# Kernel optimization log

Hardware: AMD Instinct MI355X
Metric: run time of the kernel (lower is better)

The kernel has to match this reference:

```python
import jax, jax.numpy as jnp
import numpy as np
from jax import lax

H = 128; N = 32768; D = 16; B = 256; E2 = N * D; L = 2; NC = 10
NPG = N // B  # nodes per graph


def _ln(x, g, b):
    m = jnp.mean(x, -1, keepdims=True)
    v = jnp.mean((x - m) ** 2, -1, keepdims=True)
    return (x - m) * lax.rsqrt(v + 1e-5) * g + b


def _lrelu(x):
    return jnp.where(x >= 0, x, 0.01 * x)


def _seg_mean(x, ids):
    s = jax.ops.segment_sum(x, ids, num_segments=B)
    c = jax.ops.segment_sum(jnp.ones((x.shape[0], 1), x.dtype), ids, num_segments=B)
    return s / c


def _lstm_agg(seq, Wih, Whh, bih, bhh):
    # seq: [N, D, H] neighbor message sequences; returns final hidden [N, H]
    n = seq.shape[0]
    h0 = jnp.zeros((n, H), seq.dtype)

    def step(carry, x):
        h, c = carry
        g = x @ Wih.T + bih + h @ Whh.T + bhh  # [N, 4H], gate order i,f,g,o (torch LSTM)
        i, f, gg, o = jnp.split(g, 4, axis=-1)
        c = jax.nn.sigmoid(f) * c + jax.nn.sigmoid(i) * jnp.tanh(gg)
        h = jax.nn.sigmoid(o) * jnp.tanh(c)
        return (h, c), None

    (h, _), _ = lax.scan(step, (h0, h0), jnp.swapaxes(seq, 0, 1))
    return h


def _gru(x, h, Wih, Whh, bih, bhh):
    gi = x @ Wih.T + bih
    gh = h @ Whh.T + bhh
    ir, iz, inn = jnp.split(gi, 3, axis=-1)
    hr, hz, hn = jnp.split(gh, 3, axis=-1)
    r = jax.nn.sigmoid(ir + hr)
    z = jax.nn.sigmoid(iz + hz)
    nn_ = jnp.tanh(inn + r * hn)
    return (1.0 - z) * nn_ + z * h


def _sage(fs, fd, nbr, Wih, Whh, bih, bhh, fsW, fsb, fnW, fnb):
    # SAGEConv with LSTM aggregator: fc_self(dst) + fc_neigh(lstm over neighbor feats)
    hn = _lstm_agg(fs[nbr], Wih, Whh, bih, bhh)  # [N, H]
    return fd @ fsW.T + fsb + hn @ fnW.T + fnb


def _forward(ints, fl):
    (act_ids, dur_ids, act2_ids, nbr_a2d, nbr_d2a, src2, dst2, graph_ids) = ints
    (emb_act, emb_dur, emb_act2, transform_W, transform_b,
     ggc_W, ggc_b, gru_Wih, gru_Whh, gru_bih, gru_bhh, hn_g, hn_b,
     lstm_Wih, lstm_Whh, lstm_bih, lstm_bhh, fcs_W, fcs_b, fcn_W, fcn_b,
     n1_g, n1_b, n3_g, n3_b,
     mh_W1, mh_b1, mh_W2, mh_b2, mo_W1, mo_b1, mo_W2, mo_b2,
     mlp_W1, mlp_b1, mlp_W2, mlp_b2, cls_W, cls_b) = fl

    # embedding lookups (dropout layers are identity in eval mode)
    h_act = emb_act[act_ids]
    h_dur = emb_dur[dur_ids]
    h_g2 = emb_act2[act2_ids]
    h_new = jnp.concatenate([h_g2, h_dur], axis=1) @ transform_W.T + transform_b

    # homo branch: GatedGraphConv (n_steps=2, 1 etype) + residual + LN + leaky_relu
    res = h_new
    hh = h_new
    for _ in range(2):
        m = hh @ ggc_W.T + ggc_b
        a = jax.ops.segment_sum(m[src2], dst2, num_segments=N)
        hh = _gru(a, hh, gru_Wih, gru_Whh, gru_bih, gru_bhh)
    h_new = _lrelu(_ln(hh + res, hn_g, hn_b))
    hg2_mean = _seg_mean(h_new, graph_ids)  # [B, H]

    # hetero branch: L layers of HeteroGraphConv(SAGEConv lstm) + norms + residuals
    ha, hd = h_act, h_dur
    for l in range(L):
        nd = _sage(ha, hd, nbr_a2d, lstm_Wih[l, 0], lstm_Whh[l, 0], lstm_bih[l, 0], lstm_bhh[l, 0],
                   fcs_W[l, 0], fcs_b[l, 0], fcn_W[l, 0], fcn_b[l, 0])
        na = _sage(hd, ha, nbr_d2a, lstm_Wih[l, 1], lstm_Whh[l, 1], lstm_bih[l, 1], lstm_bhh[l, 1],
                   fcs_W[l, 1], fcs_b[l, 1], fcn_W[l, 1], fcn_b[l, 1])
        na = _lrelu(_ln(na, n1_g[l, 0], n1_b[l, 0]))
        nd = _lrelu(_ln(nd, n1_g[l, 1], n1_b[l, 1]))
        ha = _lrelu(_ln(ha + na, n3_g[l, 0], n3_b[l, 0]))
        hd = _lrelu(_ln(hd + nd, n3_g[l, 1], n3_b[l, 1]))
    hg_mean = _seg_mean(ha, graph_ids) + _seg_mean(hd, graph_ids)  # sum over ntypes

    o1 = jax.nn.relu(jax.nn.relu(hg2_mean @ mo_W1.T + mo_b1) @ mo_W2.T + mo_b2)
    o2 = jax.nn.relu(jax.nn.relu(hg_mean @ mh_W1.T + mh_b1) @ mh_W2.T + mh_b2)
    hc = jnp.concatenate([o1, hg2_mean, o2, hg_mean], axis=1)  # [B, 4H]
    preds = jax.nn.relu(jax.nn.relu(hc @ mlp_W1.T + mlp_b1) @ mlp_W2.T + mlp_b2)
    return preds @ cls_W.T + cls_b  # [B, NC]


def setup_inputs() -> dict:
    key = jax.random.key(0)
    ks = iter(jax.random.split(key, 48))
    s = 1.0 / np.sqrt(H)

    def nrm(shape, sc=s):
        return jax.random.normal(next(ks), shape, jnp.float32) * sc

    inp = {}
    inp['act_ids'] = jax.random.randint(next(ks), (N,), 0, 30)
    inp['dur_ids'] = jax.random.randint(next(ks), (N,), 0, 1024)
    inp['act2_ids'] = jax.random.randint(next(ks), (N,), 0, 30)
    inp['nbr_a2d'] = jax.random.randint(next(ks), (N, D), 0, N)
    inp['nbr_d2a'] = jax.random.randint(next(ks), (N, D), 0, N)
    inp['src2'] = jax.random.randint(next(ks), (E2,), 0, N)
    inp['dst2'] = jax.random.randint(next(ks), (E2,), 0, N)
    inp['graph_ids'] = jnp.arange(N) // NPG

    inp['emb_act'] = nrm((30, H))
    inp['emb_dur'] = nrm((1024, H))
    inp['emb_act2'] = nrm((30, H))
    inp['transform_W'] = nrm((H, 2 * H), 1.0 / np.sqrt(2 * H))
    inp['transform_b'] = jnp.zeros((H,), jnp.float32)
    inp['ggc_W'] = nrm((H, H))
    inp['ggc_b'] = jnp.zeros((H,), jnp.float32)
    inp['gru_Wih'] = nrm((3 * H, H))
    inp['gru_Whh'] = nrm((3 * H, H))
    inp['gru_bih'] = jnp.zeros((3 * H,), jnp.float32)
    inp['gru_bhh'] = jnp.zeros((3 * H,), jnp.float32)
    inp['hn_g'] = jnp.ones((H,), jnp.float32)
    inp['hn_b'] = jnp.zeros((H,), jnp.float32)
    inp['lstm_Wih'] = nrm((L, 2, 4 * H, H))
    inp['lstm_Whh'] = nrm((L, 2, 4 * H, H))
    inp['lstm_bih'] = jnp.zeros((L, 2, 4 * H), jnp.float32)
    inp['lstm_bhh'] = jnp.zeros((L, 2, 4 * H), jnp.float32)
    inp['fcs_W'] = nrm((L, 2, H, H))
    inp['fcs_b'] = jnp.zeros((L, 2, H), jnp.float32)
    inp['fcn_W'] = nrm((L, 2, H, H))
    inp['fcn_b'] = jnp.zeros((L, 2, H), jnp.float32)
    inp['n1_g'] = jnp.ones((L, 2, H), jnp.float32)
    inp['n1_b'] = jnp.zeros((L, 2, H), jnp.float32)
    inp['n3_g'] = jnp.ones((L, 2, H), jnp.float32)
    inp['n3_b'] = jnp.zeros((L, 2, H), jnp.float32)
    inp['mh_W1'] = nrm((H, H)); inp['mh_b1'] = jnp.zeros((H,), jnp.float32)
    inp['mh_W2'] = nrm((H, H)); inp['mh_b2'] = jnp.zeros((H,), jnp.float32)
    inp['mo_W1'] = nrm((H, H)); inp['mo_b1'] = jnp.zeros((H,), jnp.float32)
    inp['mo_W2'] = nrm((H, H)); inp['mo_b2'] = jnp.zeros((H,), jnp.float32)
    inp['mlp_W1'] = nrm((2 * H, 4 * H), 1.0 / np.sqrt(4 * H))
    inp['mlp_b1'] = jnp.zeros((2 * H,), jnp.float32)
    inp['mlp_W2'] = nrm((H, 2 * H), 1.0 / np.sqrt(2 * H))
    inp['mlp_b2'] = jnp.zeros((H,), jnp.float32)
    inp['cls_W'] = nrm((NC, H))
    inp['cls_b'] = jnp.zeros((NC,), jnp.float32)
    return inp


def reference(act_ids, dur_ids, act2_ids, nbr_a2d, nbr_d2a, src2, dst2, graph_ids,
              emb_act, emb_dur, emb_act2, transform_W, transform_b,
              ggc_W, ggc_b, gru_Wih, gru_Whh, gru_bih, gru_bhh, hn_g, hn_b,
              lstm_Wih, lstm_Whh, lstm_bih, lstm_bhh, fcs_W, fcs_b, fcn_W, fcn_b,
              n1_g, n1_b, n3_g, n3_b,
              mh_W1, mh_b1, mh_W2, mh_b2, mo_W1, mo_b1, mo_W2, mo_b2,
              mlp_W1, mlp_b1, mlp_W2, mlp_b2, cls_W, cls_b):
    ints = (act_ids, dur_ids, act2_ids, nbr_a2d, nbr_d2a, src2, dst2, graph_ids)
    fl = (emb_act, emb_dur, emb_act2, transform_W, transform_b,
          ggc_W, ggc_b, gru_Wih, gru_Whh, gru_bih, gru_bhh, hn_g, hn_b,
          lstm_Wih, lstm_Whh, lstm_bih, lstm_bhh, fcs_W, fcs_b, fcn_W, fcn_b,
          n1_g, n1_b, n3_g, n3_b,
          mh_W1, mh_b1, mh_W2, mh_b2, mo_W1, mo_b1, mo_W2, mo_b2,
          mlp_W1, mlp_b1, mlp_W2, mlp_b2, cls_W, cls_b)
    return _forward(ints, fl)
```

## Files before the change

kernel.cpp:

```cpp
#include <hip/hip_runtime.h>
#include <hip/hip_fp16.h>
#include <math.h>

#define NN 32768
#define HH 128
#define DD 16
#define BB 256
#define E2N (NN*DD)
#define NF (NN*HH)

typedef __attribute__((ext_vector_type(4))) float f32x4;
typedef __attribute__((ext_vector_type(4))) unsigned short u16x4;
typedef __attribute__((ext_vector_type(8))) unsigned short u16x8;
typedef _Float16 f16x8 __attribute__((ext_vector_type(8)));

__device__ __forceinline__ float fsig(float x) {
  return __builtin_amdgcn_rcpf(1.0f + __builtin_amdgcn_exp2f(-1.442695041f*x));
}
__device__ __forceinline__ float ftanh(float x) {
  return 1.0f - 2.0f*__builtin_amdgcn_rcpf(1.0f + __builtin_amdgcn_exp2f(2.885390082f*x));
}
__device__ __forceinline__ void hsplit(float x, unsigned short& h, unsigned short& l) {
  __half hh_ = __float2half_rn(x);
  h = __half_as_ushort(hh_);
  l = __half_as_ushort(__float2half_rn(x - __half2float(hh_)));
}

struct TDesc { const float* src; float* dst; int R; int C; };
struct TDescArr { TDesc d[8]; };

__global__ void transpose_many(TDescArr da) {
  TDesc t = da.d[blockIdx.y];
  int idx = blockIdx.x*256 + threadIdx.x;
  if (idx < t.R*t.C) {
    int r = idx / t.C, c = idx - r*t.C;
    t.dst[(size_t)c*t.R + r] = t.src[idx];
  }
}

__global__ void bias_sum_kernel(const float* __restrict__ bih, const float* __restrict__ bhh,
                                float* __restrict__ bsum) {
  int i = blockIdx.x*256 + threadIdx.x;
  if (i < 2048) bsum[i] = bih[i] + bhh[i];
}

__global__ void f32to16_kernel(const float* __restrict__ in, unsigned short* __restrict__ out) {
  int base = (blockIdx.x*256 + threadIdx.x) * 4;
  float4 v = *(const float4*)(in + base);
  u16x4 p;
  p[0] = __half_as_ushort(__float2half_rn(v.x));
  p[1] = __half_as_ushort(__float2half_rn(v.y));
  p[2] = __half_as_ushort(__float2half_rn(v.z));
  p[3] = __half_as_ushort(__float2half_rn(v.w));
  *(u16x4*)(out + base) = p;
}

__global__ void wsplit16_kernel(const float* __restrict__ W,
                                unsigned short* __restrict__ hi,
                                unsigned short* __restrict__ lo) {
  int i = blockIdx.x*256 + threadIdx.x;
  unsigned short h, l;
  hsplit(W[i], h, l);
  hi[i] = h; lo[i] = l;
}

__global__ void embed3_kernel(const int* __restrict__ a_ids, const int* __restrict__ d_ids,
                              const int* __restrict__ a2_ids,
                              const float* __restrict__ ea, const float* __restrict__ ed,
                              const float* __restrict__ ea2,
                              float* __restrict__ ha, float* __restrict__ hd,
                              float* __restrict__ hg2) {
  int idx = blockIdx.x*256 + threadIdx.x;
  int n = idx >> 7, j = idx & 127;
  int w = blockIdx.y;
  if (w == 0)      ha[idx]  = ea[(size_t)a_ids[n]*128 + j];
  else if (w == 1) hd[idx]  = ed[(size_t)d_ids[n]*128 + j];
  else             hg2[idx] = ea2[(size_t)a2_ids[n]*128 + j];
}

template<int BN, int ACT>
__global__ __launch_bounds__(256) void gemm_nt(
    const float* __restrict__ A0, const float* __restrict__ A1,
    const float* __restrict__ A2, const float* __restrict__ A3,
    int lda, const float* __restrict__ WT, const float* __restrict__ bias,
    float* __restrict__ C, int K, int beta)
{
  extern __shared__ float sm[];
  const int KP = K + 4;
  float* At = sm;
  float* Bc = sm + 32*KP;
  const int tid = threadIdx.x;
  const int m0 = blockIdx.x*32;
  const int ng = tid >> 5, cg = tid & 31;
  const int n0 = ng*4, c4 = cg*4;
  constexpr int G = BN/128;
  float acc[G][4][4];
#pragma unroll
  for (int g=0; g<G; ++g)
#pragma unroll
    for (int i=0;i<4;++i)
#pragma unroll
      for (int e=0;e<4;++e) acc[g][i][e] = 0.0f;

  const int nf4 = K >> 2;
  for (int idx = tid; idx < 32*nf4; idx += 256) {
    int row = idx / nf4;
    int kk = (idx - row*nf4) << 2;
    const float* Ap = (kk < 128) ? A0 : (kk < 256) ? A1 : (kk < 384) ? A2 : A3;
    float4 v = *(const float4*)(Ap + (size_t)(m0+row)*lda + (kk & 127));
    *(float4*)(At + row*KP + kk) = v;
  }
  const int nchunk = K >> 4;
  for (int kc = 0; kc < nchunk; ++kc) {
    __syncthreads();
    for (int idx = tid; idx < 16*(BN/4); idx += 256) {
      int kk = idx / (BN/4);
      int jq = idx - kk*(BN/4);
      *(float4*)(Bc + kk*BN + jq*4) = *(const float4*)(WT + (size_t)(kc*16+kk)*BN + jq*4);
    }
    __syncthreads();
    for (int k=0;k<16;++k) {
      const int kk = kc*16 + k;
      float av[4];
#pragma unroll
      for (int i=0;i<4;++i) av[i] = At[(n0+i)*KP + kk];
#pragma unroll
      for (int g=0; g<G; ++g) {
        float4 bv = *(const float4*)(Bc + k*BN + g*128 + c4);
        float bb[4] = {bv.x, bv.y, bv.z, bv.w};
#pragma unroll
        for (int i=0;i<4;++i)
#pragma unroll
          for (int e=0;e<4;++e)
            acc[g][i][e] += av[i]*bb[e];
      }
    }
  }
#pragma unroll
  for (int g=0; g<G; ++g) {
#pragma unroll
    for (int i=0;i<4;++i) {
      float* dst = C + (size_t)(m0+n0+i)*BN + g*128 + c4;
      float o[4];
#pragma unroll
      for (int e=0;e<4;++e) o[e] = acc[g][i][e];
      if (bias) {
#pragma unroll
        for (int e=0;e<4;++e) o[e] += bias[g*128 + c4 + e];
      }
      if (beta) {
        float4 p = *(const float4*)dst;
        o[0]+=p.x; o[1]+=p.y; o[2]+=p.z; o[3]+=p.w;
      }
      if (ACT==1) {
#pragma unroll
        for (int e=0;e<4;++e) o[e] = fmaxf(o[e], 0.0f);
      }
      *(float4*)dst = make_float4(o[0],o[1],o[2],o[3]);
    }
  }
}

__device__ __forceinline__ void stage_hi_lo(const float* __restrict__ A, int rb, int tid,
                                            unsigned short* xhi, unsigned short* xlo) {
  const int r = tid >> 3;
  const int cf = (tid & 7) * 16;
  const float* src = A + (size_t)(rb + r)*128 + cf;
  unsigned short* dh = xhi + r*136 + cf;
  unsigned short* dl = xlo + r*136 + cf;
#pragma unroll
  for (int q=0; q<4; ++q) {
    float4 v = *(const float4*)(src + q*4);
    float vs[4] = {v.x, v.y, v.z, v.w};
    u16x4 ph, pl;
#pragma unroll
    for (int e=0;e<4;++e){ unsigned short h_,l_; hsplit(vs[e],h_,l_); ph[e]=h_; pl[e]=l_; }
    *(u16x4*)(dh + q*4) = ph;
    *(u16x4*)(dl + q*4) = pl;
  }
}

__global__ __launch_bounds__(512) void mgemm(
    const float* __restrict__ A,
    const unsigned short* __restrict__ Whi, const unsigned short* __restrict__ Wlo,
    const float* __restrict__ bias, float* __restrict__ C, int BN, int ntpw)
{
  __shared__ unsigned short xhi[64*136];
  __shared__ unsigned short xlo[64*136];
  const int tid = threadIdx.x;
  const int w = tid >> 6;
  const int lane = tid & 63;
  const int ln16 = lane & 15;
  const int lq = lane >> 4;
  const int rb = blockIdx.x * 64;
  stage_hi_lo(A, rb, tid, xhi, xlo);
  __syncthreads();

  for (int j=0; j<ntpw; ++j) {
    const int tile = w + j*8;
    f32x4 acc[4];
    f32x4 bv = *(const f32x4*)(bias + tile*16 + lq*4);
#pragma unroll
    for (int nt=0; nt<4; ++nt) acc[nt] = bv;
#pragma unroll
    for (int kt=0; kt<4; ++kt) {
      const int bo = kt*32 + lq*8;
      f16x8 bxh[4], bxl[4];
#pragma unroll
      for (int nt=0; nt<4; ++nt) {
        bxh[nt] = *(const f16x8*)(xhi + (nt*16+ln16)*136 + bo);
        bxl[nt] = *(const f16x8*)(xlo + (nt*16+ln16)*136 + bo);
      }
      const size_t co = (size_t)(tile*16 + ln16)*128 + kt*32 + lq*8;
      f16x8 ah = *(const f16x8*)(Whi + co);
      f16x8 al = *(const f16x8*)(Wlo + co);
#pragma unroll
      for (int nt=0; nt<4; ++nt) {
        acc[nt] = __builtin_amdgcn_mfma_f32_16x16x32_f16(ah, bxh[nt], acc[nt], 0,0,0);
        acc[nt] = __builtin_amdgcn_mfma_f32_16x16x32_f16(ah, bxl[nt], acc[nt], 0,0,0);
        acc[nt] = __builtin_amdgcn_mfma_f32_16x16x32_f16(al, bxh[nt], acc[nt], 0,0,0);
      }
    }
#pragma unroll
    for (int nt=0; nt<4; ++nt) {
      f32x4 o = acc[nt];
      *(float4*)(C + (size_t)(rb + nt*16 + ln16)*BN + tile*16 + lq*4) =
          make_float4(o[0],o[1],o[2],o[3]);
    }
  }
}

__global__ __launch_bounds__(512) void mgemm2(
    const float* __restrict__ A1,
    const unsigned short* __restrict__ W1hi, const unsigned short* __restrict__ W1lo,
    const float* __restrict__ A2,
    const unsigned short* __restrict__ W2hi, const unsigned short* __restrict__ W2lo,
    const float* __restrict__ bias1, const float* __restrict__ bias2,
    float* __restrict__ C, int wstride)
{
  extern __shared__ unsigned short sm16[];
  unsigned short* x1hi = sm16;
  unsigned short* x1lo = sm16 + 8704;
  unsigned short* x2hi = sm16 + 17408;
  unsigned short* x2lo = sm16 + 26112;
  const int tid = threadIdx.x;
  const int w = tid >> 6;
  const int lane = tid & 63;
  const int ln16 = lane & 15;
  const int lq = lane >> 4;
  const int rb = blockIdx.x * 64;
  stage_hi_lo(A1, rb, tid, x1hi, x1lo);
  stage_hi_lo(A2, rb, tid, x2hi, x2lo);
  __syncthreads();

  f32x4 acc[4];
  {
    f32x4 bv = *(const f32x4*)(bias1 + w*16 + lq*4);
    if (bias2) {
      f32x4 b2 = *(const f32x4*)(bias2 + w*16 + lq*4);
#pragma unroll
      for (int e=0;e<4;++e) bv[e] += b2[e];
    }
#pragma unroll
    for (int nt=0; nt<4; ++nt) acc[nt] = bv;
  }
#pragma unroll
  for (int p=0; p<2; ++p) {
    const unsigned short* xh = p ? x2hi : x1hi;
    const unsigned short* xl = p ? x2lo : x1lo;
    const unsigned short* Wh = p ? W2hi : W1hi;
    const unsigned short* Wl = p ? W2lo : W1lo;
#pragma unroll
    for (int kt=0; kt<4; ++kt) {
      const int bo = kt*32 + lq*8;
      f16x8 bxh[4], bxl[4];
#pragma unroll
      for (int nt=0; nt<4; ++nt) {
        bxh[nt] = *(const f16x8*)(xh + (nt*16+ln16)*136 + bo);
        bxl[nt] = *(const f16x8*)(xl + (nt*16+ln16)*136 + bo);
      }
      const size_t co = (size_t)(w*16 + ln16)*wstride + kt*32 + lq*8;
      f16x8 ah = *(const f16x8*)(Wh + co);
      f16x8 al = *(const f16x8*)(Wl + co);
#pragma unroll
      for (int nt=0; nt<4; ++nt) {
        acc[nt] = __builtin_amdgcn_mfma_f32_16x16x32_f16(ah, bxh[nt], acc[nt], 0,0,0);
        acc[nt] = __builtin_amdgcn_mfma_f32_16x16x32_f16(ah, bxl[nt], acc[nt], 0,0,0);
        acc[nt] = __builtin_amdgcn_mfma_f32_16x16x32_f16(al, bxh[nt], acc[nt], 0,0,0);
      }
    }
  }
#pragma unroll
  for (int nt=0; nt<4; ++nt) {
    f32x4 o = acc[nt];
    *(float4*)(C + (size_t)(rb + nt*16 + ln16)*128 + w*16 + lq*4) =
        make_float4(o[0],o[1],o[2],o[3]);
  }
}

__global__ __launch_bounds__(512) void gru_fused(
    const float* __restrict__ abuf, float* __restrict__ hh,
    const unsigned short* __restrict__ GIhi, const unsigned short* __restrict__ GIlo,
    const unsigned short* __restrict__ GHhi, const unsigned short* __restrict__ GHlo,
    const float* __restrict__ bih, const float* __restrict__ bhh)
{
  extern __shared__ unsigned short sm16[];
  unsigned short* xhi = sm16;
  unsigned short* xlo = sm16 + 8704;
  unsigned short* hhi = sm16 + 17408;
  unsigned short* hlo = sm16 + 26112;
  const int tid = threadIdx.x;
  const int w = tid >> 6;
  const int lane = tid & 63;
  const int ln16 = lane & 15;
  const int lq = lane >> 4;
  const int rb = blockIdx.x * 64;
  stage_hi_lo(abuf, rb, tid, xhi, xlo);
  stage_hi_lo(hh, rb, tid, hhi, hlo);
  __syncthreads();

  f32x4 rr[4], zz[4], nn_[4];
#pragma unroll
  for (int j=0; j<3; ++j) {
    const int tile = w + j*8;
    f32x4 ai[4], ag[4];
    f32x4 bi = *(const f32x4*)(bih + tile*16 + lq*4);
    f32x4 bg = *(const f32x4*)(bhh + tile*16 + lq*4);
#pragma unroll
    for (int nt=0; nt<4; ++nt) { ai[nt] = bi; ag[nt] = bg; }
#pragma unroll
    for (int kt=0; kt<4; ++kt) {
      const int bo = kt*32 + lq*8;
      f16x8 bxh[4], bxl[4], bhh_[4], bhl_[4];
#pragma unroll
      for (int nt=0; nt<4; ++nt) {
        bxh[nt] = *(const f16x8*)(xhi + (nt*16+ln16)*136 + bo);
        bxl[nt] = *(const f16x8*)(xlo + (nt*16+ln16)*136 + bo);
        bhh_[nt] = *(const f16x8*)(hhi + (nt*16+ln16)*136 + bo);
        bhl_[nt] = *(const f16x8*)(hlo + (nt*16+ln16)*136 + bo);
      }
      const size_t co = (size_t)(tile*16 + ln16)*128 + kt*32 + lq*8;
      f16x8 ih = *(const f16x8*)(GIhi + co);
      f16x8 il = *(const f16x8*)(GIlo + co);
      f16x8 gh = *(const f16x8*)(GHhi + co);
      f16x8 gl = *(const f16x8*)(GHlo + co);
#pragma unroll
      for (int nt=0; nt<4; ++nt) {
        ai[nt] = __builtin_amdgcn_mfma_f32_16x16x32_f16(ih, bxh[nt], ai[nt], 0,0,0);
        ai[nt] = __builtin_amdgcn_mfma_f32_16x16x32_f16(ih, bxl[nt], ai[nt], 0,0,0);
        ai[nt] = __builtin_amdgcn_mfma_f32_16x16x32_f16(il, bxh[nt], ai[nt], 0,0,0);
        ag[nt] = __builtin_amdgcn_mfma_f32_16x16x32_f16(gh, bhh_[nt], ag[nt], 0,0,0);
        ag[nt] = __builtin_amdgcn_mfma_f32_16x16x32_f16(gh, bhl_[nt], ag[nt], 0,0,0);
        ag[nt] = __builtin_amdgcn_mfma_f32_16x16x32_f16(gl, bhh_[nt], ag[nt], 0,0,0);
      }
    }
#pragma unroll
    for (int nt=0; nt<4; ++nt) {
#pragma unroll
      for (int e=0; e<4; ++e) {
        if (j == 0)      rr[nt][e] = fsig(ai[nt][e] + ag[nt][e]);
        else if (j == 1) zz[nt][e] = fsig(ai[nt][e] + ag[nt][e]);
        else             nn_[nt][e] = ftanh(ai[nt][e] + rr[nt][e]*ag[nt][e]);
      }
    }
  }
#pragma unroll
  for (int nt=0; nt<4; ++nt) {
    float* hp = hh + (size_t)(rb + nt*16 + ln16)*128 + w*16 + lq*4;
    float4 ho = *(const float4*)hp;
    float hv[4] = {ho.x, ho.y, ho.z, ho.w};
    float o[4];
#pragma unroll
    for (int e=0; e<4; ++e)
      o[e] = (1.0f - zz[nt][e])*nn_[nt][e] + zz[nt][e]*hv[e];
    *(float4*)hp = make_float4(o[0],o[1],o[2],o[3]);
  }
}

__global__ __launch_bounds__(512) void lstm_fused6(
    float* __restrict__ hL,
    const unsigned short* __restrict__ fs16a, const unsigned short* __restrict__ fs16d,
    const int* __restrict__ nbrA, const int* __restrict__ nbrD,
    const unsigned short* __restrict__ WI0, const unsigned short* __restrict__ WH0,
    const unsigned short* __restrict__ WI1, const unsigned short* __restrict__ WH1,
    const float* __restrict__ bsum0, const float* __restrict__ bsum1)
{
  __shared__ unsigned short xb[64*132];
  __shared__ unsigned short hb[64*132];
  const int tid = threadIdx.x;
  const int w = tid >> 6;
  const int lane = tid & 63;
  const int ln16 = lane & 15;
  const int lq = lane >> 4;
  const int b = blockIdx.x;
  const bool dir = (b >= 512);
  const int nb = (dir ? (b - 512) : b) * 64;
  const unsigned short* fs16 = dir ? fs16d : fs16a;
  const int* nbr = dir ? nbrD : nbrA;
  const unsigned short* WI = dir ? WI1 : WI0;
  const unsigned short* WH = dir ? WH1 : WH0;
  const float* bsum = dir ? bsum1 : bsum0;

  const int gr = tid >> 3;
  const int gc = (tid & 7) * 16;
  const int* nrow = nbr + (size_t)(nb + gr)*DD;

  f32x4 bias[4];
#pragma unroll
  for (int g=0; g<4; ++g)
    bias[g] = *(const f32x4*)(bsum + g*128 + w*16 + lq*4);

  f32x4 cst[4];
#pragma unroll
  for (int nt=0; nt<4; ++nt)
#pragma unroll
    for (int e=0; e<4; ++e) cst[nt][e] = 0.0f;

  u16x8 xg0, xg1;
  {
    int gidx = nrow[0];
    const unsigned short* src = fs16 + (size_t)gidx*128 + gc;
    xg0 = *(const u16x8*)(src);
    xg1 = *(const u16x8*)(src + 8);
    unsigned short* d = xb + gr*132 + gc;
    *(u16x8*)d = xg0;
    *(u16x8*)(d+8) = xg1;
  }
  int gnext = nrow[1];

#pragma unroll 1
  for (int t=0; t<16; ++t) {
    __syncthreads();

    f32x4 racc[4][4];
#pragma unroll
    for (int g=0; g<4; ++g)
#pragma unroll
      for (int nt=0; nt<4; ++nt)
        racc[g][nt] = bias[g];

#pragma unroll
    for (int kt=0; kt<4; ++kt) {
      const int bo = kt*32 + lq*8;
      f16x8 bx[4];
#pragma unroll
      for (int nt=0; nt<4; ++nt)
        bx[nt] = *(const f16x8*)(xb + (nt*16+ln16)*132 + bo);
#pragma unroll
      for (int g=0; g<4; ++g) {
        f16x8 aI = *(const f16x8*)(WI + (size_t)(g*128 + w*16 + ln16)*128 + kt*32 + lq*8);
#pragma unroll
        for (int nt=0; nt<4; ++nt)
          racc[g][nt] = __builtin_amdgcn_mfma_f32_16x16x32_f16(aI, bx[nt], racc[g][nt], 0,0,0);
      }
    }
    if (t < 15) {
      const unsigned short* src = fs16 + (size_t)gnext*128 + gc;
      xg0 = *(const u16x8*)(src);
      xg1 = *(const u16x8*)(src + 8);
      if (t < 14) gnext = nrow[t+2];
    }
    if (t > 0) {
#pragma unroll
      for (int kt=0; kt<4; ++kt) {
        const int bo = kt*32 + lq*8;
        f16x8 bh[4];
#pragma unroll
        for (int nt=0; nt<4; ++nt)
          bh[nt] = *(const f16x8*)(hb + (nt*16+ln16)*132 + bo);
#pragma unroll
        for (int g=0; g<4; ++g) {
          f16x8 aH = *(const f16x8*)(WH + (size_t)(g*128 + w*16 + ln16)*128 + kt*32 + lq*8);
#pragma unroll
          for (int nt=0; nt<4; ++nt)
            racc[g][nt] = __builtin_amdgcn_mfma_f32_16x16x32_f16(aH, bh[nt], racc[g][nt], 0,0,0);
        }
      }
    }
    __syncthreads();

#pragma unroll
    for (int nt=0; nt<4; ++nt) {
      float hv[4];
#pragma unroll
      for (int e=0; e<4; ++e) {
        float ig = fsig(racc[0][nt][e]);
        float fg = fsig(racc[1][nt][e]);
        float gg = ftanh(racc[2][nt][e]);
        float og = fsig(racc[3][nt][e]);
        float cc = fg*cst[nt][e] + ig*gg;
        cst[nt][e] = cc;
        hv[e] = og*ftanh(cc);
      }
      const int node = nt*16 + ln16;
      const int col = w*16 + lq*4;
      if (t < 15) {
        u16x4 hw;
#pragma unroll
        for (int e=0; e<4; ++e) hw[e] = __half_as_ushort(__float2half_rn(hv[e]));
        *(u16x4*)(hb + node*132 + col) = hw;
      } else {
        *(float4*)(hL + (size_t)((dir?NN:0) + nb + node)*128 + col) =
            make_float4(hv[0], hv[1], hv[2], hv[3]);
      }
    }
    if (t < 15) {
      unsigned short* d = xb + gr*132 + gc;
      *(u16x8*)d = xg0;
      *(u16x8*)(d+8) = xg1;
    }
  }
}

__global__ void scatter_add_kernel(float* __restrict__ a, const float* __restrict__ m,
                                   const int* __restrict__ src, const int* __restrict__ dst) {
  int wid = (blockIdx.x*256 + threadIdx.x) >> 6;
  int lane = threadIdx.x & 63;
  int s = src[wid], d = dst[wid];
  const float* mr = m + (size_t)s*128;
  float* ar = a + (size_t)d*128;
  atomicAdd(ar + lane, mr[lane]);
  atomicAdd(ar + 64 + lane, mr[64 + lane]);
}

__global__ void ln_lrelu_kernel(float* __restrict__ out, const float* __restrict__ x,
                                const float* __restrict__ add,
                                const float* __restrict__ g, const float* __restrict__ b) {
  int n = blockIdx.x, j = threadIdx.x;
  size_t base = (size_t)n*128;
  float v = x[base+j];
  if (add) v += add[base+j];
  __shared__ float sh[4];
  float s = v;
#pragma unroll
  for (int m=32; m>=1; m>>=1) s += __shfl_xor(s, m, 64);
  if ((j&63)==0) sh[j>>6] = s;
  __syncthreads();
  float mean = (sh[0]+sh[1]) * 0.0078125f;
  float d = v - mean;
  float q = d*d;
#pragma unroll
  for (int m=32; m>=1; m>>=1) q += __shfl_xor(q, m, 64);
  if ((j&63)==0) sh[2+(j>>6)] = q;
  __syncthreads();
  float var = (sh[2]+sh[3]) * 0.0078125f;
  float y = d * rsqrtf(var + 1e-5f) * g[j] + b[j];
  out[base+j] = (y >= 0.0f) ? y : 0.01f*y;
}

__global__ void ln13_kernel(float* __restrict__ h, const float* __restrict__ nsrc,
                            const float* __restrict__ g1, const float* __restrict__ b1,
                            const float* __restrict__ g3, const float* __restrict__ b3,
                            unsigned short* __restrict__ out16) {
  int n = blockIdx.x, j = threadIdx.x;
  size_t base = (size_t)n*128;
  __shared__ float sh[4];
  float v = nsrc[base+j];
  float s = v;
#pragma unroll
  for (int m=32; m>=1; m>>=1) s += __shfl_xor(s, m, 64);
  if ((j&63)==0) sh[j>>6] = s;
  __syncthreads();
  float mean = (sh[0]+sh[1]) * 0.0078125f;
  float d = v - mean;
  float q = d*d;
#pragma unroll
  for (int m=32; m>=1; m>>=1) q += __shfl_xor(q, m, 64);
  if ((j&63)==0) sh[2+(j>>6)] = q;
  __syncthreads();
  float var = (sh[2]+sh[3]) * 0.0078125f;
  float y1 = d * rsqrtf(var + 1e-5f) * g1[j] + b1[j];
  y1 = (y1 >= 0.0f) ? y1 : 0.01f*y1;
  __syncthreads();
  float u = h[base+j] + y1;
  s = u;
#pragma unroll
  for (int m=32; m>=1; m>>=1) s += __shfl_xor(s, m, 64);
  if ((j&63)==0) sh[j>>6] = s;
  __syncthreads();
  mean = (sh[0]+sh[1]) * 0.0078125f;
  d = u - mean;
  q = d*d;
#pragma unroll
  for (int m=32; m>=1; m>>=1) q += __shfl_xor(q, m, 64);
  if ((j&63)==0) sh[2+(j>>6)] = q;
  __syncthreads();
  var = (sh[2]+sh[3]) * 0.0078125f;
  float y3 = d * rsqrtf(var + 1e-5f) * g3[j] + b3[j];
  float o = (y3 >= 0.0f) ? y3 : 0.01f*y3;
  h[base+j] = o;
  if (out16) out16[base+j] = __half_as_ushort(__float2half_rn(o));
}

__global__ void segmean_kernel(float* __restrict__ out, const float* __restrict__ x,
                               const float* __restrict__ y) {
  int b = blockIdx.x, j = threadIdx.x;
  float s = 0.0f;
  for (int r=0; r<128; ++r) {
    size_t n = (size_t)(b*128 + r)*128 + j;
    s += x[n];
    if (y) s += y[n];
  }
  out[(size_t)b*128 + j] = s * 0.0078125f;
}

__global__ void cls_kernel(float* __restrict__ out, const float* __restrict__ h2,
                           const float* __restrict__ Wc, const float* __restrict__ bc) {
  int gid = blockIdx.x*256 + threadIdx.x;
  if (gid >= BB*10) return;
  int mrow = gid/10, c = gid - mrow*10;
  const float* arow = h2 + (size_t)mrow*128;
  const float* wrow = Wc + (size_t)c*128;
  float s = bc[c];
  for (int k=0;k<128;++k) s += arow[k]*wrow[k];
  out[gid] = s;
}

__global__ void bail_kernel(float* out, float v) {
  if (threadIdx.x==0 && blockIdx.x==0) out[0] = v;
}

extern "C" void kernel_launch(void* const* d_in, const int* in_sizes, int n_in,
                              void* d_out, int out_size, void* d_ws, size_t ws_size,
                              hipStream_t stream)
{
  const int* act_ids  = (const int*)d_in[0];
  const int* dur_ids  = (const int*)d_in[1];
  const int* act2_ids = (const int*)d_in[2];
  const int* nbr_a2d  = (const int*)d_in[3];
  const int* nbr_d2a  = (const int*)d_in[4];
  const int* src2     = (const int*)d_in[5];
  const int* dst2     = (const int*)d_in[6];
  const float* emb_act     = (const float*)d_in[8];
  const float* emb_dur     = (const float*)d_in[9];
  const float* emb_act2    = (const float*)d_in[10];
  const float* transform_W = (const float*)d_in[11];
  const float* transform_b = (const float*)d_in[12];
  const float* ggc_W   = (const float*)d_in[13];
  const float* ggc_b   = (const float*)d_in[14];
  const float* gru_Wih = (const float*)d_in[15];
  const float* gru_Whh = (const float*)d_in[16];
  const float* gru_bih = (const float*)d_in[17];
  const float* gru_bhh = (const float*)d_in[18];
  const float* hn_g    = (const float*)d_in[19];
  const float* hn_b    = (const float*)d_in[20];
  const float* lstm_Wih = (const float*)d_in[21];
  const float* lstm_Whh = (const float*)d_in[22];
  const float* lstm_bih = (const float*)d_in[23];
  const float* lstm_bhh = (const float*)d_in[24];
  const float* fcs_W = (const float*)d_in[25];
  const float* fcs_b = (const float*)d_in[26];
  const float* fcn_W = (const float*)d_in[27];
  const float* fcn_b = (const float*)d_in[28];
  const float* n1_g = (const float*)d_in[29];
  const float* n1_b = (const float*)d_in[30];
  const float* n3_g = (const float*)d_in[31];
  const float* n3_b = (const float*)d_in[32];
  const float* mh_W1 = (const float*)d_in[33];
  const float* mh_b1 = (const float*)d_in[34];
  const float* mh_W2 = (const float*)d_in[35];
  const float* mh_b2 = (const float*)d_in[36];
  const float* mo_W1 = (const float*)d_in[37];
  const float* mo_b1 = (const float*)d_in[38];
  const float* mo_W2 = (const float*)d_in[39];
  const float* mo_b2 = (const float*)d_in[40];
  const float* mlp_W1 = (const float*)d_in[41];
  const float* mlp_b1 = (const float*)d_in[42];
  const float* mlp_W2 = (const float*)d_in[43];
  const float* mlp_b2 = (const float*)d_in[44];
  const float* cls_W = (const float*)d_in[45];
  const float* cls_b = (const float*)d_in[46];

  float* ws = (float*)d_ws;
  float* ha   = ws;
  float* hd   = ws + (size_t)NF;
  float* hg2  = ws + 2*(size_t)NF;
  float* res  = ws + 3*(size_t)NF;
  float* hh   = ws + 4*(size_t)NF;
  float* SCR  = ws + 5*(size_t)NF;
  float* mb   = SCR;
  float* abuf = SCR + (size_t)NF;
  float* hnf  = mb;
  float* hLb  = SCR + 8*(size_t)NF;
  float* SMALL = ws + 15*(size_t)NF;
  float* hg2m = SMALL;
  float* hgm  = SMALL + 32768;
  float* o1b  = SMALL + 65536;
  float* o2b  = SMALL + 98304;
  float* t1b  = SMALL + 131072;
  float* t2b  = SMALL + 163840;
  float* h1b  = SMALL + 196608;
  float* h2b  = SMALL + 262144;
  float* bsum = SMALL + 294912;
  float* WTb  = SMALL + 296960;
  const size_t NEED_BYTES = (size_t)(15*(size_t)NF + 296960 + 1032192) * 4;
  if (ws_size < NEED_BYTES) {
    hipMemsetAsync(d_out, 0, (size_t)out_size*sizeof(float), stream);
    bail_kernel<<<1,64,0,stream>>>((float*)d_out, (float)ws_size);
    return;
  }
  float* na = hg2;
  float* nd = res;
  unsigned short* fs16a = (unsigned short*)(SCR + 2*(size_t)NF);
  unsigned short* fs16d = fs16a + (size_t)NF;

  const int O_TRANSFORM = 0;
  const int O_SPLIT    = 147456;
  const int O_SPLIT2   = 409600;
  const int O_MH1      = 802816;
  const int O_MH2      = 819200;
  const int O_MO1      = 835584;
  const int O_MO2      = 851968;
  const int O_MLP1     = 868352;
  const int O_MLP2     = 999424;

  unsigned short* THi = (unsigned short*)(WTb + O_TRANSFORM);
  unsigned short* TLo = THi + 32768;
  unsigned short* WI16 = (unsigned short*)(WTb + O_SPLIT);
  unsigned short* WH16 = WI16 + 4*65536;

  unsigned short* SP2 = (unsigned short*)(WTb + O_SPLIT2);
  unsigned short* GGChi = SP2;                 unsigned short* GGClo = GGChi + 16384;
  unsigned short* GIHhi = GGClo + 16384;       unsigned short* GIHlo = GIHhi + 49152;
  unsigned short* GHHhi = GIHlo + 49152;       unsigned short* GHHlo = GHHhi + 49152;
  unsigned short* FCShi = GHHlo + 49152;       unsigned short* FCSlo = FCShi + 65536;
  unsigned short* FCNhi = FCSlo + 65536;       unsigned short* FCNlo = FCNhi + 65536;

  TDescArr da;
  int di = 0;
  auto addT = [&](const float* s, float* d, int R, int C){ da.d[di].src=s; da.d[di].dst=d; da.d[di].R=R; da.d[di].C=C; ++di; };
  addT(mh_W1, WTb + O_MH1, 128, 128);
  addT(mh_W2, WTb + O_MH2, 128, 128);
  addT(mo_W1, WTb + O_MO1, 128, 128);
  addT(mo_W2, WTb + O_MO2, 128, 128);
  addT(mlp_W1, WTb + O_MLP1, 256, 512);
  addT(mlp_W2, WTb + O_MLP2, 128, 256);
  transpose_many<<<dim3(512, di), 256, 0, stream>>>(da);
  bias_sum_kernel<<<8, 256, 0, stream>>>(lstm_bih, lstm_bhh, bsum);
  f32to16_kernel<<<(4*512*128)/1024, 256, 0, stream>>>(lstm_Wih, WI16);
  f32to16_kernel<<<(4*512*128)/1024, 256, 0, stream>>>(lstm_Whh, WH16);
  wsplit16_kernel<<<32768/256, 256, 0, stream>>>(transform_W, THi, TLo);
  wsplit16_kernel<<<16384/256, 256, 0, stream>>>(ggc_W, GGChi, GGClo);
  wsplit16_kernel<<<49152/256, 256, 0, stream>>>(gru_Wih, GIHhi, GIHlo);
  wsplit16_kernel<<<49152/256, 256, 0, stream>>>(gru_Whh, GHHhi, GHHlo);
  wsplit16_kernel<<<65536/256, 256, 0, stream>>>(fcs_W, FCShi, FCSlo);
  wsplit16_kernel<<<65536/256, 256, 0, stream>>>(fcn_W, FCNhi, FCNlo);

  auto smemK = [](int K, int BN){ return (size_t)(32*(K+4) + 16*BN)*4; };
  const int gB = BB/32;
  const int gM = NN/64;
  const size_t LDS2 = 69632;

  embed3_kernel<<<dim3(NF/256, 3), 256, 0, stream>>>(act_ids, dur_ids, act2_ids,
      emb_act, emb_dur, emb_act2, ha, hd, hg2);
  mgemm2<<<gM, 512, LDS2, stream>>>(hg2, THi, TLo, hd, THi + 128, TLo + 128,
      transform_b, nullptr, res, 256);
  hipMemcpyAsync(hh, res, (size_t)NF*4, hipMemcpyDeviceToDevice, stream);

  for (int it=0; it<2; ++it) {
    mgemm<<<gM, 512, 0, stream>>>(hh, GGChi, GGClo, ggc_b, mb, 128, 1);
    hipMemsetAsync(abuf, 0, (size_t)NF*4, stream);
    scatter_add_kernel<<<E2N/4, 256, 0, stream>>>(abuf, mb, src2, dst2);
    gru_fused<<<gM, 512, LDS2, stream>>>(abuf, hh, GIHhi, GIHlo, GHHhi, GHHlo,
        gru_bih, gru_bhh);
  }
  ln_lrelu_kernel<<<NN, 128, 0, stream>>>(hnf, hh, res, hn_g, hn_b);
  segmean_kernel<<<BB, 128, 0, stream>>>(hg2m, hnf, nullptr);

  f32to16_kernel<<<NF/1024, 256, 0, stream>>>(ha, fs16a);
  f32to16_kernel<<<NF/1024, 256, 0, stream>>>(hd, fs16d);

  for (int l=0; l<2; ++l) {
    const int i0 = l*2 + 0, i1 = l*2 + 1;
    lstm_fused6<<<1024, 512, 0, stream>>>(hLb, fs16a, fs16d, nbr_a2d, nbr_d2a,
        WI16 + i0*65536, WH16 + i0*65536,
        WI16 + i1*65536, WH16 + i1*65536,
        bsum + i0*512, bsum + i1*512);

    mgemm2<<<gM, 512, LDS2, stream>>>(hd, FCShi + i0*16384, FCSlo + i0*16384,
        hLb, FCNhi + i0*16384, FCNlo + i0*16384,
        fcs_b + i0*128, fcn_b + i0*128, nd, 128);
    mgemm2<<<gM, 512, LDS2, stream>>>(ha, FCShi + i1*16384, FCSlo + i1*16384,
        hLb + (size_t)NN*128, FCNhi + i1*16384, FCNlo + i1*16384,
        fcs_b + i1*128, fcn_b + i1*128, na, 128);
    ln13_kernel<<<NN, 128, 0, stream>>>(ha, na, n1_g + i0*128, n1_b + i0*128,
        n3_g + i0*128, n3_b + i0*128, (l==0) ? fs16a : nullptr);
    ln13_kernel<<<NN, 128, 0, stream>>>(hd, nd, n1_g + i1*128, n1_b + i1*128,
        n3_g + i1*128, n3_b + i1*128, (l==0) ? fs16d : nullptr);
  }
  segmean_kernel<<<BB, 128, 0, stream>>>(hgm, ha, hd);

  gemm_nt<128,1><<<gB, 256, smemK(128,128), stream>>>(hg2m, nullptr, nullptr, nullptr, 128,
      WTb + O_MO1, mo_b1, t1b, 128, 0);
  gemm_nt<128,1><<<gB, 256, smemK(128,128), stream>>>(t1b, nullptr, nullptr, nullptr, 128,
      WTb + O_MO2, mo_b2, o1b, 128, 0);
  gemm_nt<128,1><<<gB, 256, smemK(128,128), stream>>>(hgm, nullptr, nullptr, nullptr, 128,
      WTb + O_MH1, mh_b1, t2b, 128, 0);
  gemm_nt<128,1><<<gB, 256, smemK(128,128), stream>>>(t2b, nullptr, nullptr, nullptr, 128,
      WTb + O_MH2, mh_b2, o2b, 128, 0);
  gemm_nt<256,0><<<gB, 256, smemK(256,256), stream>>>(o1b, hg2m, nullptr, nullptr, 128,
      WTb + O_MLP1, nullptr, h1b, 256, 0);
  gemm_nt<256,1><<<gB, 256, smemK(256,256), stream>>>(o2b, hgm, nullptr, nullptr, 128,
      WTb + O_MLP1 + 256*256, mlp_b1, h1b, 256, 1);
  gemm_nt<128,1><<<gB, 256, smemK(256,128), stream>>>(h1b, h1b + 128, nullptr, nullptr, 256,
      WTb + O_MLP2, mlp_b2, h2b, 256, 0);
  cls_kernel<<<10, 256, 0, stream>>>((float*)d_out, h2b, cls_W, cls_b);
}
```

Measured before the change: 1.924 ms.

## Replace atomic scatter-add with CSR gather and fuse fp16 conversions into embed

Builds a CSR (histogram, scan, fill) over the GGC edge destinations once per call. Each of the two message-passing iterations then uses a per-node gather instead of a memset plus atomic scatter-add. The fp16 feature copies are now written directly in the embedding kernel, and the transform GEMM writes its output twice, removing a device memcpy and two conversion kernels. The cost is extra preprocessing launches, including a single-block scan, and nondeterministic edge order inside each node's sum.

Result: faster. 1.625 ms (-15.5%).

```diff
diff --git a/kernel.cpp b/kernel.cpp
--- a/kernel.cpp
+++ b/kernel.cpp
@@ -64,18 +64,81 @@
   hi[i] = h; lo[i] = l;
 }
 
+__global__ void hist_kernel(const int* __restrict__ dst, int* __restrict__ cnt) {
+  int e = blockIdx.x*256 + threadIdx.x;
+  atomicAdd(&cnt[dst[e]], 1);
+}
+
+__global__ __launch_bounds__(1024) void scan_kernel(const int* __restrict__ cnt,
+                                                    int* __restrict__ rowptr,
+                                                    int* __restrict__ cursor) {
+  __shared__ int part[1024];
+  const int t = threadIdx.x;
+  const int base = t*32;
+  int loc[32];
+  int s = 0;
+#pragma unroll
+  for (int k=0;k<32;++k){ loc[k]=s; s += cnt[base+k]; }
+  part[t] = s;
+  __syncthreads();
+  for (int off=1; off<1024; off<<=1) {
+    int v = (t>=off) ? part[t-off] : 0;
+    __syncthreads();
+    part[t] += v;
+    __syncthreads();
+  }
+  int pbase = part[t] - s;
+#pragma unroll
+  for (int k=0;k<32;++k){ int v = pbase + loc[k]; rowptr[base+k]=v; cursor[base+k]=v; }
+  if (t == 1023) rowptr[NN] = part[1023];
+}
+
+__global__ void fill_kernel(const int* __restrict__ src, const int* __restrict__ dst,
+                            int* __restrict__ cursor, int* __restrict__ elist) {
+  int e = blockIdx.x*256 + threadIdx.x;
+  int p = atomicAdd(&cursor[dst[e]], 1);
+  elist[p] = src[e];
+}
+
+__global__ __launch_bounds__(256) void gather_ggc(const float* __restrict__ m,
+    const int* __restrict__ rowptr, const int* __restrict__ elist,
+    float* __restrict__ a) {
+  const int node = blockIdx.x*4 + (threadIdx.x>>6);
+  const int lane = threadIdx.x & 63;
+  const int s0 = rowptr[node], s1 = rowptr[node+1];
+  float a0 = 0.0f, a1 = 0.0f;
+  for (int e=s0; e<s1; ++e) {
+    const float* mr = m + (size_t)elist[e]*128;
+    a0 += mr[lane];
+    a1 += mr[64+lane];
+  }
+  float* ar = a + (size_t)node*128;
+  ar[lane] = a0;
+  ar[64+lane] = a1;
+}
+
 __global__ void embed3_kernel(const int* __restrict__ a_ids, const int* __restrict__ d_ids,
                               const int* __restrict__ a2_ids,
                               const float* __restrict__ ea, const float* __restrict__ ed,
                               const float* __restrict__ ea2,
                               float* __restrict__ ha, float* __restrict__ hd,
-                              float* __restrict__ hg2) {
+                              float* __restrict__ hg2,
+                              unsigned short* __restrict__ fs16a,
+                              unsigned short* __restrict__ fs16d) {
   int idx = blockIdx.x*256 + threadIdx.x;
   int n = idx >> 7, j = idx & 127;
   int w = blockIdx.y;
-  if (w == 0)      ha[idx]  = ea[(size_t)a_ids[n]*128 + j];
-  else if (w == 1) hd[idx]  = ed[(size_t)d_ids[n]*128 + j];
-  else             hg2[idx] = ea2[(size_t)a2_ids[n]*128 + j];
+  if (w == 0) {
+    float v = ea[(size_t)a_ids[n]*128 + j];
+    ha[idx] = v;
+    fs16a[idx] = __half_as_ushort(__float2half_rn(v));
+  } else if (w == 1) {
+    float v = ed[(size_t)d_ids[n]*128 + j];
+    hd[idx] = v;
+    fs16d[idx] = __half_as_ushort(__float2half_rn(v));
+  } else {
+    hg2[idx] = ea2[(size_t)a2_ids[n]*128 + j];
+  }
 }
 
 template<int BN, int ACT>
@@ -236,7 +299,7 @@
     const float* __restrict__ A2,
     const unsigned short* __restrict__ W2hi, const unsigned short* __restrict__ W2lo,
     const float* __restrict__ bias1, const float* __restrict__ bias2,
-    float* __restrict__ C, int wstride)
+    float* __restrict__ C, float* __restrict__ C2, int wstride)
 {
   extern __shared__ unsigned short sm16[];
   unsigned short* x1hi = sm16;
@@ -293,8 +356,9 @@
 #pragma unroll
   for (int nt=0; nt<4; ++nt) {
     f32x4 o = acc[nt];
-    *(float4*)(C + (size_t)(rb + nt*16 + ln16)*128 + w*16 + lq*4) =
-        make_float4(o[0],o[1],o[2],o[3]);
+    const size_t off = (size_t)(rb + nt*16 + ln16)*128 + w*16 + lq*4;
+    *(float4*)(C + off) = make_float4(o[0],o[1],o[2],o[3]);
+    if (C2) *(float4*)(C2 + off) = make_float4(o[0],o[1],o[2],o[3]);
   }
 }
 
@@ -510,17 +574,6 @@
       *(u16x8*)(d+8) = xg1;
     }
   }
-}
-
-__global__ void scatter_add_kernel(float* __restrict__ a, const float* __restrict__ m,
-                                   const int* __restrict__ src, const int* __restrict__ dst) {
-  int wid = (blockIdx.x*256 + threadIdx.x) >> 6;
-  int lane = threadIdx.x & 63;
-  int s = src[wid], d = dst[wid];
-  const float* mr = m + (size_t)s*128;
-  float* ar = a + (size_t)d*128;
-  atomicAdd(ar + lane, mr[lane]);
-  atomicAdd(ar + 64 + lane, mr[64 + lane]);
 }
 
 __global__ void ln_lrelu_kernel(float* __restrict__ out, const float* __restrict__ x,
@@ -703,6 +756,10 @@
   float* nd = res;
   unsigned short* fs16a = (unsigned short*)(SCR + 2*(size_t)NF);
   unsigned short* fs16d = fs16a + (size_t)NF;
+  int* csr_cnt    = (int*)(SCR + 3*(size_t)NF);
+  int* csr_rowptr = csr_cnt + NN;
+  int* csr_cursor = csr_rowptr + NN + 2;
+  int* csr_elist  = csr_cursor + NN;
 
   const int O_TRANSFORM = 0;
   const int O_SPLIT    = 147456;
@@ -745,6 +802,10 @@
   wsplit16_kernel<<<49152/256, 256, 0, stream>>>(gru_Whh, GHHhi, GHHlo);
   wsplit16_kernel<<<65536/256, 256, 0, stream>>>(fcs_W, FCShi, FCSlo);
   wsplit16_kernel<<<65536/256, 256, 0, stream>>>(fcn_W, FCNhi, FCNlo);
+  hipMemsetAsync(csr_cnt, 0, (size_t)NN*sizeof(int), stream);
+  hist_kernel<<<E2N/256, 256, 0, stream>>>(dst2, csr_cnt);
+  scan_kernel<<<1, 1024, 0, stream>>>(csr_cnt, csr_rowptr, csr_cursor);
+  fill_kernel<<<E2N/256, 256, 0, stream>>>(src2, dst2, csr_cursor, csr_elist);
 
   auto smemK = [](int K, int BN){ return (size_t)(32*(K+4) + 16*BN)*4; };
   const int gB = BB/32;
@@ -752,23 +813,18 @@
   const size_t LDS2 = 69632;
 
   embed3_kernel<<<dim3(NF/256, 3), 256, 0, stream>>>(act_ids, dur_ids, act2_ids,
-      emb_act, emb_dur, emb_act2, ha, hd, hg2);
+      emb_act, emb_dur, emb_act2, ha, hd, hg2, fs16a, fs16d);
   mgemm2<<<gM, 512, LDS2, stream>>>(hg2, THi, TLo, hd, THi + 128, TLo + 128,
-      transform_b, nullptr, res, 256);
-  hipMemcpyAsync(hh, res, (size_t)NF*4, hipMemcpyDeviceToDevice, stream);
+      transform_b, nullptr, res, hh, 256);
 
   for (int it=0; it<2; ++it) {
     mgemm<<<gM, 512, 0, stream>>>(hh, GGChi, GGClo, ggc_b, mb, 128, 1);
-    hipMemsetAsync(abuf, 0, (size_t)NF*4, stream);
-    scatter_add_kernel<<<E2N/4, 256, 0, stream>>>(abuf, mb, src2, dst2);
+    gather_ggc<<<NN/4, 256, 0, stream>>>(mb, csr_rowptr, csr_elist, abuf);
     gru_fused<<<gM, 512, LDS2, stream>>>(abuf, hh, GIHhi, GIHlo, GHHhi, GHHlo,
         gru_bih, gru_bhh);
   }
   ln_lrelu_kernel<<<NN, 128, 0, stream>>>(hnf, hh, res, hn_g, hn_b);
   segmean_kernel<<<BB, 128, 0, stream>>>(hg2m, hnf, nullptr);
-
-  f32to16_kernel<<<NF/1024, 256, 0, stream>>>(ha, fs16a);
-  f32to16_kernel<<<NF/1024, 256, 0, stream>>>(hd, fs16d);
 
   for (int l=0; l<2; ++l) {
     const int i0 = l*2 + 0, i1 = l*2 + 1;
@@ -779,10 +835,10 @@
 
     mgemm2<<<gM, 512, LDS2, stream>>>(hd, FCShi + i0*16384, FCSlo + i0*16384,
         hLb, FCNhi + i0*16384, FCNlo + i0*16384,
-        fcs_b + i0*128, fcn_b + i0*128, nd, 128);
+        fcs_b + i0*128, fcn_b + i0*128, nd, nullptr, 128);
     mgemm2<<<gM, 512, LDS2, stream>>>(ha, FCShi + i1*16384, FCSlo + i1*16384,
         hLb + (size_t)NN*128, FCNhi + i1*16384, FCNlo + i1*16384,
-        fcs_b + i1*128, fcn_b + i1*128, na, 128);
+        fcs_b + i1*128, fcn_b + i1*128, na, nullptr, 128);
     ln13_kernel<<<NN, 128, 0, stream>>>(ha, na, n1_g + i0*128, n1_b + i0*128,
         n3_g + i0*128, n3_b + i0*128, (l==0) ? fs16a : nullptr);
     ln13_kernel<<<NN, 128, 0, stream>>>(hd, nd, n1_g + i1*128, n1_b + i1*128,
```
